# Kernel tuning notes

Measured on AMD Instinct MI355X. Metric: run time of the kernel, lower is better.

## Reference

```python
import jax, jax.numpy as jnp
import numpy as np

NUM_HEADS = 16
HEAD_DIM = 64
TOP_K_TILES = 8
TILE_SIZE = 16
ROPE_BASE = 10000.0


def make_freqs_cis(seq_len, head_dim):
    # [seq, head_dim//2] complex64, standard RoPE frequencies
    inv_freq = 1.0 / (ROPE_BASE ** (jnp.arange(0, head_dim, 2, dtype=jnp.float32) / head_dim))
    angles = jnp.arange(seq_len, dtype=jnp.float32)[:, None] * inv_freq[None, :]
    return jax.lax.complex(jnp.cos(angles), jnp.sin(angles))


def apply_rope(xq, xk, freqs_cis):
    # xq, xk: [b, h, s, d]; pairs adjacent channels as (real, imag)
    xq_ = xq.astype(jnp.float32).reshape(*xq.shape[:-1], -1, 2)
    xk_ = xk.astype(jnp.float32).reshape(*xk.shape[:-1], -1, 2)
    xq_c = jax.lax.complex(xq_[..., 0], xq_[..., 1])
    xk_c = jax.lax.complex(xk_[..., 0], xk_[..., 1])
    f = freqs_cis[None, None, :xq.shape[2], :]
    xq_r = xq_c * f
    xk_r = xk_c * f
    xq_out = jnp.stack([xq_r.real, xq_r.imag], axis=-1).reshape(xq.shape)
    xk_out = jnp.stack([xk_r.real, xk_r.imag], axis=-1).reshape(xk.shape)
    return xq_out.astype(xq.dtype), xk_out.astype(xk.dtype)


def setup_inputs() -> dict:
    key = jax.random.key(0)
    ks = jax.random.split(key, 5)
    B, S, D = 2, 2048, 1024
    scale = 1.0 / np.sqrt(D)
    return {
        "x": jax.random.normal(ks[0], (B, S, D), dtype=jnp.float32),
        "wq": jax.random.normal(ks[1], (D, NUM_HEADS * HEAD_DIM), dtype=jnp.float32) * scale,
        "wk": jax.random.normal(ks[2], (D, NUM_HEADS * HEAD_DIM), dtype=jnp.float32) * scale,
        "wv": jax.random.normal(ks[3], (D, NUM_HEADS * HEAD_DIM), dtype=jnp.float32) * scale,
        "wo": jax.random.normal(ks[4], (NUM_HEADS * HEAD_DIM, D), dtype=jnp.float32) * scale,
    }


def reference(x, wq, wk, wv, wo):
    batch, seq_len, _ = x.shape
    q = (x @ wq).reshape(batch, seq_len, NUM_HEADS, HEAD_DIM)
    k = (x @ wk).reshape(batch, seq_len, NUM_HEADS, HEAD_DIM)
    v = (x @ wv).reshape(batch, seq_len, NUM_HEADS, HEAD_DIM)

    freqs_cis = make_freqs_cis(seq_len, HEAD_DIM)
    q_t = jnp.transpose(q, (0, 2, 1, 3))
    k_t = jnp.transpose(k, (0, 2, 1, 3))
    q_t, k_t = apply_rope(q_t, k_t, freqs_cis)
    q = jnp.transpose(q_t, (0, 2, 1, 3))
    k = jnp.transpose(k_t, (0, 2, 1, 3))

    logits = jnp.einsum('bqhd,bkhd->bhqk', q, k) / jnp.sqrt(jnp.float32(HEAD_DIM))
    causal = jnp.tril(jnp.ones((seq_len, seq_len), dtype=bool))
    logits = jnp.where(causal[None, None, :, :], logits, -1e10)
    weights = jax.nn.softmax(logits, axis=-1)  # [b, h, q, k]

    # Scout: tile-max-pool last token's attention probs + top-k tile selection
    last_token_probs = weights[:, :, -1, :]  # [b, h, k]
    pad_len = (TILE_SIZE - seq_len % TILE_SIZE) % TILE_SIZE
    if pad_len > 0:
        last_token_probs = jnp.pad(last_token_probs, ((0, 0), (0, 0), (0, pad_len)))
    num_tiles = last_token_probs.shape[-1] // TILE_SIZE
    tile_scores = jnp.max(
        last_token_probs.reshape(batch, NUM_HEADS, num_tiles, TILE_SIZE), axis=-1)
    _, top_tile_indices = jax.lax.top_k(tile_scores, TOP_K_TILES)  # [b, h, top_k]

    output = jnp.einsum('bhqk,bkhd->bqhd', weights, v)
    output = output.reshape(batch, seq_len, NUM_HEADS * HEAD_DIM)
    output = output @ wo
    return output, top_tile_indices
```

## Files before the change

kernel.cpp:

```cpp
#include <hip/hip_runtime.h>

#define B_ 2
#define S_ 2048
#define E_ 1024
#define H_ 16
#define D_ 64
#define BS_ (B_*S_)
#define PSTR 76

typedef unsigned short u16;
typedef __attribute__((ext_vector_type(8))) short short8;
typedef __attribute__((ext_vector_type(4))) float floatx4;
typedef __bf16 bf16x8 __attribute__((ext_vector_type(8)));

__device__ __forceinline__ u16 f2bf(float f) {
    unsigned int u = __builtin_bit_cast(unsigned int, f);
    u += 0x7FFFu + ((u >> 16) & 1u);
    return (u16)(u >> 16);
}
__device__ __forceinline__ float bf2f(u16 h) {
    return __builtin_bit_cast(float, (unsigned int)h << 16);
}
__device__ __forceinline__ floatx4 mfma16(short8 a, short8 b, floatx4 c) {
    return __builtin_amdgcn_mfma_f32_16x16x32_bf16(
        __builtin_bit_cast(bf16x8, a), __builtin_bit_cast(bf16x8, b), c, 0, 0, 0);
}
__device__ __forceinline__ void gload_lds16(const void* g, void* l) {
    __builtin_amdgcn_global_load_lds(
        (const __attribute__((address_space(1))) unsigned int*)g,
        (__attribute__((address_space(3))) unsigned int*)l, 16, 0, 0);
}

__global__ __launch_bounds__(256) void prep_kernel(const float* __restrict__ x,
                                                   const float* __restrict__ wq,
                                                   const float* __restrict__ wk,
                                                   const float* __restrict__ wv,
                                                   const float* __restrict__ wo,
                                                   u16* __restrict__ xcat,
                                                   u16* __restrict__ wqt,
                                                   u16* __restrict__ wkt,
                                                   u16* __restrict__ wkres,
                                                   u16* __restrict__ wvt,
                                                   u16* __restrict__ wot,
                                                   float* __restrict__ cost,
                                                   float* __restrict__ sint,
                                                   float* __restrict__ qlast) {
    __shared__ float t[32][33];
    int bx = blockIdx.x;
    int tid = threadIdx.x;
    if (bx < 4096) {
        int i = bx * 256 + tid;
        int row = i >> 8, c4 = (i & 255) * 4;
        float4 v = ((const float4*)x)[i];
        u16 h0 = f2bf(v.x), h1 = f2bf(v.y), h2 = f2bf(v.z), h3 = f2bf(v.w);
        uint2 o;
        o.x = (unsigned)h0 | ((unsigned)h1 << 16);
        o.y = (unsigned)h2 | ((unsigned)h3 << 16);
        *(uint2*)&xcat[(size_t)row * 2048 + c4] = o;
        u16 l0 = f2bf(v.x - bf2f(h0)), l1 = f2bf(v.y - bf2f(h1));
        u16 l2 = f2bf(v.z - bf2f(h2)), l3 = f2bf(v.w - bf2f(h3));
        uint2 ol;
        ol.x = (unsigned)l0 | ((unsigned)l1 << 16);
        ol.y = (unsigned)l2 | ((unsigned)l3 << 16);
        *(uint2*)&xcat[(size_t)row * 2048 + 1024 + c4] = ol;
    } else if (bx < 8192) {
        int sub = bx - 4096;
        int which = sub >> 10, s2 = sub & 1023;
        const float* W = which == 0 ? wq : which == 1 ? wk : which == 2 ? wv : wo;
        u16* Wt = which == 0 ? wqt : which == 1 ? wkt : which == 2 ? wvt : wot;
        int tk = (s2 >> 5) * 32, tn = (s2 & 31) * 32;
        int tx = tid & 31, ty = tid >> 5;
        for (int i = 0; i < 32; i += 8)
            t[ty + i][tx] = W[(size_t)(tk + ty + i) * E_ + tn + tx];
        __syncthreads();
        for (int i = 0; i < 32; i += 8) {
            float v = t[tx][ty + i];
            u16 hi = f2bf(v);
            Wt[(size_t)(tn + ty + i) * E_ + tk + tx] = hi;
            if (which == 1) {
                wkres[(size_t)(tn + ty + i) * 2048 + tk + tx] = f2bf(v - bf2f(hi));
                wkres[(size_t)(tn + ty + i) * 2048 + 1024 + tk + tx] = hi;
            }
        }
    } else if (bx < 8448) {
        int idx = (bx - 8192) * 256 + tid;
        int s = idx >> 5, i = idx & 31;
        float inv = powf(10000.0f, -(float)i / 32.0f);
        float a = (float)s * inv;
        cost[idx] = cosf(a);
        sint[idx] = sinf(a);
    } else {
        float* red = &t[0][0];
        int b2 = bx - 8448;
        int b = b2 >> 5, c0 = (b2 & 31) * 32;
        int cl = tid & 31, kc = tid >> 5;
        const float* xr = &x[((size_t)b * S_ + (S_ - 1)) * E_ + kc * 128];
        const float* wp = &wq[(size_t)(kc * 128) * E_ + c0 + cl];
        float acc = 0.f;
#pragma unroll 4
        for (int e = 0; e < 128; ++e) acc = fmaf(xr[e], wp[(size_t)e * E_], acc);
        red[kc * 32 + cl] = acc;
        __syncthreads();
        if (kc == 0) {
            float s = ((red[0 * 32 + cl] + red[1 * 32 + cl]) + (red[2 * 32 + cl] + red[3 * 32 + cl]))
                    + ((red[4 * 32 + cl] + red[5 * 32 + cl]) + (red[6 * 32 + cl] + red[7 * 32 + cl]));
            qlast[(size_t)b * E_ + c0 + cl] = s;
        }
    }
}


__device__ __forceinline__ void stage_swz(const u16* __restrict__ src, int row0, int k0,
                                          int stride, u16* lds, int tid) {
    int wv = tid >> 6, ln = tid & 63;
    int swz = (((ln & 7) ^ (ln >> 3)) << 3);
    int rr = ln >> 3;
#pragma unroll
    for (int i = 0; i < 4; ++i) {
        int seg = i * 4 + wv;
        gload_lds16(&src[(size_t)(row0 + seg * 8 + rr) * stride + k0 + swz],
                    (char*)lds + (size_t)seg * 1024);
    }
}

__device__ __forceinline__ void gemm_body(const u16* lA, const u16* lB,
                                          floatx4 (*acc)[4], int lane, int wave) {
    int wm = (wave >> 1) * 64, wn = (wave & 1) * 64;
    int lr = lane & 15, lq = lane >> 4, r7 = lr & 7;
#pragma unroll
    for (int half = 0; half < 2; ++half) {
        int xo = (((half * 4 + lq) ^ r7) << 3);
        short8 afr[4], bfr[4];
#pragma unroll
        for (int mi = 0; mi < 4; ++mi)
            afr[mi] = *(const short8*)&lA[(wm + mi * 16 + lr) * 64 + xo];
#pragma unroll
        for (int ni = 0; ni < 4; ++ni)
            bfr[ni] = *(const short8*)&lB[(wn + ni * 16 + lr) * 64 + xo];
        __builtin_amdgcn_s_setprio(1);
#pragma unroll
        for (int mi = 0; mi < 4; ++mi)
#pragma unroll
            for (int ni = 0; ni < 4; ++ni)
                acc[mi][ni] = mfma16(afr[mi], bfr[ni], acc[mi][ni]);
        __builtin_amdgcn_s_setprio(0);
    }
}

__device__ __forceinline__ void gemm_write(float* __restrict__ C, floatx4 (*acc)[4],
                                           int m0, int n0, int N, int lane, int wave) {
    int wm = (wave >> 1) * 64, wn = (wave & 1) * 64;
    int lr = lane & 15, lq = lane >> 4;
#pragma unroll
    for (int mi = 0; mi < 4; ++mi)
#pragma unroll
        for (int ni = 0; ni < 4; ++ni)
#pragma unroll
            for (int r = 0; r < 4; ++r)
                C[(size_t)(m0 + wm + mi * 16 + lq * 4 + r) * N + n0 + wn + ni * 16 + lr]
                    = acc[mi][ni][r];
}

__device__ __forceinline__ void rope_epilogue(floatx4 (*acc)[4], int m0, int n0,
                                              const float* __restrict__ cost,
                                              const float* __restrict__ sint,
                                              const float* __restrict__ qlast,
                                              u16* __restrict__ dstb,
                                              float* __restrict__ tscores,
                                              int lane, int wave) {
    int wm = (wave >> 1) * 64, wn = (wave & 1) * 64;
    int lr = lane & 15, lq = lane >> 4;
    int odd = lr & 1;
    int h = (n0 + wn) >> 6;
    int bq = m0 >> 11;
    int s0 = m0 & 2047;
    float qr[4];
    if (qlast) {
#pragma unroll
        for (int ni = 0; ni < 4; ++ni) {
            int d = ni * 16 + lr;
            int i = d >> 1;
            float qv = qlast[(size_t)bq * E_ + h * 64 + d];
            float qp = __shfl_xor(qv, 1);
            float c = cost[2047 * 32 + i], sn = sint[2047 * 32 + i];
            qr[ni] = odd ? (qp * sn + qv * c) : (qv * c - qp * sn);
        }
    }
    float dotp[4][4];
#pragma unroll
    for (int mi = 0; mi < 4; ++mi)
#pragma unroll
        for (int r = 0; r < 4; ++r) dotp[mi][r] = 0.f;
#pragma unroll
    for (int ni = 0; ni < 4; ++ni) {
        int d = ni * 16 + lr;
        int i = d >> 1;
#pragma unroll
        for (int mi = 0; mi < 4; ++mi) {
#pragma unroll
            for (int r = 0; r < 4; ++r) {
                int row = m0 + wm + mi * 16 + lq * 4 + r;
                int s = row & 2047;
                float own = acc[mi][ni][r];
                float par = __shfl_xor(own, 1);
                float c = cost[s * 32 + i], sn = sint[s * 32 + i];
                float out = odd ? (par * sn + own * c) : (own * c - par * sn);
                dstb[(((size_t)(bq * 16 + h)) * S_ + s) * 64 + d] = f2bf(out);
                if (qlast) dotp[mi][r] += out * qr[ni];
            }
        }
    }
    if (qlast) {
#pragma unroll
        for (int mi = 0; mi < 4; ++mi) {
            float tm = -1e30f;
#pragma unroll
            for (int r = 0; r < 4; ++r) {
                float dv = dotp[mi][r];
                dv += __shfl_xor(dv, 1);
                dv += __shfl_xor(dv, 2);
                dv += __shfl_xor(dv, 4);
                dv += __shfl_xor(dv, 8);
                tm = fmaxf(tm, dv);
            }
            tm = fmaxf(tm, __shfl_xor(tm, 16));
            tm = fmaxf(tm, __shfl_xor(tm, 32));
            if (lane == 0)
                tscores[(size_t)(bq * 16 + h) * 128 + (s0 >> 4) + (wm >> 4) + mi] = tm;
        }
    }
}

__device__ __forceinline__ void v_epilogue(floatx4 (*acc)[4], int m0, int n0,
                                           u16* vt, u16* __restrict__ vtb,
                                           int lane, int wave, int tid) {
    int wm = (wave >> 1) * 64, wn = (wave & 1) * 64;
    int lr = lane & 15, lq = lane >> 4;
#pragma unroll
    for (int ni = 0; ni < 4; ++ni) {
        int dcol = wn + ni * 16 + lr;
#pragma unroll
        for (int mi = 0; mi < 4; ++mi)
#pragma unroll
            for (int r = 0; r < 4; ++r)
                vt[dcol * 136 + wm + mi * 16 + lq * 4 + r] = f2bf(acc[mi][ni][r]);
    }
    __syncthreads();
    int dcol = tid >> 1, sh = (tid & 1) * 64;
    int colg = n0 + dcol, h = colg >> 6, d = colg & 63;
    int bq = m0 >> 11, s0 = m0 & 2047;
    size_t base = (((size_t)(bq * 16 + h)) * 64 + d) * S_ + s0 + sh;
#pragma unroll
    for (int c = 0; c < 8; ++c)
        *(uint4*)&vtb[base + c * 8] = *(const uint4*)&vt[dcol * 136 + sh + c * 8];
}

__global__ __launch_bounds__(256) void proj_gemm_kernel(const u16* __restrict__ xcat,
                                                        const u16* __restrict__ wqt,
                                                        const u16* __restrict__ wkt,
                                                        const u16* __restrict__ wkres,
                                                        const u16* __restrict__ wvt,
                                                        const float* __restrict__ cost,
                                                        const float* __restrict__ sint,
                                                        const float* __restrict__ qlast,
                                                        u16* __restrict__ qb,
                                                        u16* __restrict__ kb,
                                                        float* __restrict__ tscores,
                                                        u16* __restrict__ vtb) {
    __shared__ __align__(16) u16 lsbuf[17408];
    u16* lA = lsbuf;
    u16* lB = lsbuf + 8192;
    int bx = blockIdx.x;
    int role = bx >> 8;
    int idx = bx & 255;
    int xcd = idx & 7, loc = idx >> 3;
    int m0 = (xcd * 4 + (loc & 3)) * 128;
    int n0 = (loc >> 2) * 128;
    int tid = threadIdx.x, lane = tid & 63, wave = tid >> 6;

    floatx4 acc[4][4];
#pragma unroll
    for (int i = 0; i < 4; ++i)
#pragma unroll
        for (int j = 0; j < 4; ++j) acc[i][j] = (floatx4){0.f, 0.f, 0.f, 0.f};

    if (role == 0) {
        for (int k0 = 0; k0 < 1024; k0 += 64) {
            stage_swz(xcat, m0, k0, 2048, lA, tid);
            stage_swz(wkt, n0, k0, 1024, lB, tid);
            __syncthreads();
            gemm_body(lA, lB, acc, lane, wave);
            __syncthreads();
        }
        for (int k0 = 0; k0 < 2048; k0 += 64) {
            stage_swz(xcat, m0, k0, 2048, lA, tid);
            stage_swz(wkres, n0, k0, 2048, lB, tid);
            __syncthreads();
            gemm_body(lA, lB, acc, lane, wave);
            __syncthreads();
        }
        rope_epilogue(acc, m0, n0, cost, sint, qlast, kb, tscores, lane, wave);
    } else if (role == 1) {
        for (int k0 = 0; k0 < 1024; k0 += 64) {
            stage_swz(xcat, m0, k0, 2048, lA, tid);
            stage_swz(wqt, n0, k0, 1024, lB, tid);
            __syncthreads();
            gemm_body(lA, lB, acc, lane, wave);
            __syncthreads();
        }
        rope_epilogue(acc, m0, n0, cost, sint, (const float*)nullptr, qb,
                      (float*)nullptr, lane, wave);
    } else {
        for (int k0 = 0; k0 < 1024; k0 += 64) {
            stage_swz(xcat, m0, k0, 2048, lA, tid);
            stage_swz(wvt, n0, k0, 1024, lB, tid);
            __syncthreads();
            gemm_body(lA, lB, acc, lane, wave);
            __syncthreads();
        }
        v_epilogue(acc, m0, n0, lsbuf, vtb, lane, wave, tid);
    }
}

__global__ __launch_bounds__(256) void gemm_bf16_kernel(const u16* __restrict__ A,
                                                        const u16* __restrict__ Bt,
                                                        float* __restrict__ C,
                                                        int M, int N, int Kd) {
    __shared__ __align__(16) u16 lds4[4 * 8192];
    u16* T0 = lds4;
    u16* T1 = lds4 + 8192;
    u16* T2 = lds4 + 16384;
    u16* T3 = lds4 + 24576;
    int nwg = (M / 128) * (N / 128);
    int bx = blockIdx.x;
    int q = nwg >> 3, rr = nwg & 7, xcd = bx & 7, pos = bx >> 3;
    int lbx = (xcd < rr ? xcd * (q + 1) : rr * (q + 1) + (xcd - rr) * q) + pos;
    int nbn = N / 128;
    int m0 = (lbx / nbn) * 128, n0 = (lbx % nbn) * 128;
    int tid = threadIdx.x, lane = tid & 63, wave = tid >> 6;

    floatx4 acc[4][4];
#pragma unroll
    for (int i = 0; i < 4; ++i)
#pragma unroll
        for (int j = 0; j < 4; ++j) acc[i][j] = (floatx4){0.f, 0.f, 0.f, 0.f};

    int nsteps = Kd / 64;
    stage_swz(A, m0, 0, Kd, T0, tid);
    stage_swz(Bt, n0, 0, Kd, T2, tid);
    asm volatile("s_waitcnt vmcnt(0)" ::: "memory");
    __syncthreads();
    for (int step = 0; step < nsteps; ++step) {
        int buf = step & 1;
        u16* Ac = buf ? T1 : T0;
        u16* Bc = buf ? T3 : T2;
        if (step + 1 < nsteps) {
            stage_swz(A, m0, (step + 1) * 64, Kd, buf ? T0 : T1, tid);
            stage_swz(Bt, n0, (step + 1) * 64, Kd, buf ? T2 : T3, tid);
        }
        gemm_body(Ac, Bc, acc, lane, wave);
        asm volatile("s_waitcnt vmcnt(0)" ::: "memory");
        __syncthreads();
    }
    gemm_write(C, acc, m0, n0, N, lane, wave);
}

__device__ __forceinline__ void stage_kv(const u16* __restrict__ K, const u16* __restrict__ V,
                                         int n0, u16* kbuf, u16* vbuf, int wave, int lane) {
    int lr = lane & 15, lq = lane >> 4;
    if (wave < 2) {
#pragma unroll
        for (int i = 0; i < 4; ++i) {
            int sk = wave * 4 + i;
            int kt = sk >> 1, kh = (sk & 1) * 32;
            gload_lds16(&K[(size_t)(n0 + kt * 16 + lr) * D_ + kh + lq * 8],
                        kbuf + sk * 512);
        }
    } else {
#pragma unroll
        for (int i = 0; i < 4; ++i) {
            int sv = (wave - 2) * 4 + i;
            int c = sv >> 2, o = sv & 3;
            gload_lds16(&V[(size_t)(o * 16 + lr) * S_ + n0 + c * 32 + lq * 8],
                        vbuf + sv * 512);
        }
    }
}

__global__ __launch_bounds__(256) void flash_kernel(const u16* __restrict__ qb,
                                                    const u16* __restrict__ kb,
                                                    const u16* __restrict__ vtb,
                                                    u16* __restrict__ ab) {
    __shared__ __align__(16) u16 kls[2][8 * 512];
    __shared__ __align__(16) u16 vls[2][8 * 512];
    __shared__ __align__(16) u16 ldsP[4][16 * PSTR];
    int tid = threadIdx.x;
    int lane = tid & 63, wave = tid >> 6;
    int bx = blockIdx.x;
    int xcd = bx & 7, ii = bx >> 3;
    int hid = xcd + 8 * (ii & 3);
    int qc = 31 - (ii >> 2);
    int qt0 = qc * 64 + wave * 16;
    const u16* Q = qb + (size_t)hid * S_ * D_;
    const u16* K = kb + (size_t)hid * S_ * D_;
    const u16* V = vtb + (size_t)hid * D_ * S_;
    u16* lp = &ldsP[wave][0];
    int lr = lane & 15, lq = lane >> 4, lk = lq * 8;

    short8 qfr0 = *(const short8*)&Q[(size_t)(qt0 + lr) * D_ + lk];
    short8 qfr1 = *(const short8*)&Q[(size_t)(qt0 + lr) * D_ + 32 + lk];

    floatx4 o0 = {0,0,0,0}, o1 = {0,0,0,0}, o2 = {0,0,0,0}, o3 = {0,0,0,0};
    float m = -1e30f, l = 0.f;

    stage_kv(K, V, 0, kls[0], vls[0], wave, lane);
    asm volatile("s_waitcnt vmcnt(0)" ::: "memory");
    __syncthreads();

    for (int it = 0; it <= qc; ++it) {
        int n0 = it * 64;
        int buf = it & 1;
        const u16* kbuf = kls[buf];
        const u16* vbuf = vls[buf];
        if (it < qc)
            stage_kv(K, V, n0 + 64, kls[buf ^ 1], vls[buf ^ 1], wave, lane);

        short8 ka0[4], ka1[4];
#pragma unroll
        for (int kt = 0; kt < 4; ++kt) {
            ka0[kt] = *(const short8*)&kbuf[(kt * 2 + 0) * 512 + lane * 8];
            ka1[kt] = *(const short8*)&kbuf[(kt * 2 + 1) * 512 + lane * 8];
        }
        floatx4 st[4];
#pragma unroll
        for (int kt = 0; kt < 4; ++kt) st[kt] = (floatx4){0.f, 0.f, 0.f, 0.f};
        __builtin_amdgcn_s_setprio(1);
#pragma unroll
        for (int kt = 0; kt < 4; ++kt) {
            st[kt] = mfma16(ka0[kt], qfr0, st[kt]);
            st[kt] = mfma16(ka1[kt], qfr1, st[kt]);
        }
        __builtin_amdgcn_s_setprio(0);

        const float SC = 0.18033688011112042f;
        int rem = qt0 + 16 - n0;
        float sv[4][4];
        float bmax = -1e30f;
        if (rem >= 80) {
#pragma unroll
            for (int kt = 0; kt < 4; ++kt)
#pragma unroll
                for (int r = 0; r < 4; ++r) {
                    float s = st[kt][r] * SC;
                    sv[kt][r] = s;
                    bmax = fmaxf(bmax, s);
                }
        } else {
#pragma unroll
            for (int kt = 0; kt < 4; ++kt)
#pragma unroll
                for (int r = 0; r < 4; ++r) {
                    int k = n0 + kt * 16 + lq * 4 + r;
                    float s = (k <= qt0 + lr) ? st[kt][r] * SC : -1e30f;
                    sv[kt][r] = s;
                    bmax = fmaxf(bmax, s);
                }
        }
        bmax = fmaxf(bmax, __shfl_xor(bmax, 16));
        bmax = fmaxf(bmax, __shfl_xor(bmax, 32));
        if (!__all(bmax <= m + 8.0f)) {
            float mn = fmaxf(m, bmax);
            float alpha = __builtin_amdgcn_exp2f(m - mn);
            m = mn;
            l *= alpha;
            float af[4];
#pragma unroll
            for (int r = 0; r < 4; ++r) af[r] = __shfl(alpha, lq * 4 + r);
#pragma unroll
            for (int r = 0; r < 4; ++r) {
                o0[r] *= af[r]; o1[r] *= af[r]; o2[r] *= af[r]; o3[r] *= af[r];
            }
        }
        float ps = 0.f;
#pragma unroll
        for (int kt = 0; kt < 4; ++kt) {
            float p0 = __builtin_amdgcn_exp2f(sv[kt][0] - m);
            float p1 = __builtin_amdgcn_exp2f(sv[kt][1] - m);
            float p2 = __builtin_amdgcn_exp2f(sv[kt][2] - m);
            float p3 = __builtin_amdgcn_exp2f(sv[kt][3] - m);
            ps += (p0 + p1) + (p2 + p3);
            unsigned wlo, whi;
            asm("v_cvt_pk_bf16_f32 %0, %1, %2" : "=v"(wlo) : "v"(p0), "v"(p1));
            asm("v_cvt_pk_bf16_f32 %0, %1, %2" : "=v"(whi) : "v"(p2), "v"(p3));
            *(uint2*)&lp[lr * PSTR + kt * 16 + lq * 4] = (uint2){wlo, whi};
        }
        ps += __shfl_xor(ps, 16);
        ps += __shfl_xor(ps, 32);
        l += ps;

        short8 vv[2][4];
#pragma unroll
        for (int c = 0; c < 2; ++c)
#pragma unroll
            for (int o = 0; o < 4; ++o)
                vv[c][o] = *(const short8*)&vbuf[(c * 4 + o) * 512 + lane * 8];
        asm volatile("s_waitcnt lgkmcnt(0)" ::: "memory");
        __builtin_amdgcn_s_setprio(1);
#pragma unroll
        for (int c = 0; c < 2; ++c) {
            uint2 plo = *(const uint2*)&lp[lr * PSTR + c * 32 + lk];
            uint2 phi = *(const uint2*)&lp[lr * PSTR + c * 32 + lk + 4];
            short8 pfr = __builtin_bit_cast(short8, (uint4){plo.x, plo.y, phi.x, phi.y});
            o0 = mfma16(pfr, vv[c][0], o0);
            o1 = mfma16(pfr, vv[c][1], o1);
            o2 = mfma16(pfr, vv[c][2], o2);
            o3 = mfma16(pfr, vv[c][3], o3);
        }
        __builtin_amdgcn_s_setprio(0);

        if (it < qc) {
            asm volatile("s_waitcnt vmcnt(0)" ::: "memory");
            __syncthreads();
        }
    }
    float li[4];
#pragma unroll
    for (int r = 0; r < 4; ++r) li[r] = 1.0f / __shfl(l, lq * 4 + r);
    int b = hid >> 4, h = hid & 15;
    size_t orow_base = ((size_t)b * S_ + qt0 + lq * 4) * E_ + h * D_;
#pragma unroll
    for (int r = 0; r < 4; ++r) {
        size_t rb = orow_base + (size_t)r * E_;
        ab[rb + 0  + lr] = f2bf(o0[r] * li[r]);
        ab[rb + 16 + lr] = f2bf(o1[r] * li[r]);
        ab[rb + 32 + lr] = f2bf(o2[r] * li[r]);
        ab[rb + 48 + lr] = f2bf(o3[r] * li[r]);
    }
}

__global__ __launch_bounds__(64) void topk_select_kernel(const float* __restrict__ tscores,
                                                         float* __restrict__ oidx) {
    int bh = blockIdx.x, tid = threadIdx.x;
    float v0 = tscores[bh * 128 + tid], v1 = tscores[bh * 128 + 64 + tid];
    float va, vb; int ia, ib;
    if (v1 > v0) { va = v1; ia = tid + 64; vb = v0; ib = tid; }
    else         { va = v0; ia = tid;      vb = v1; ib = tid + 64; }
    float cv = va; int ci = ia; int used = 0;
    for (int t = 0; t < 8; ++t) {
        float bv = cv; int bi = ci;
#pragma unroll
        for (int mk = 1; mk < 64; mk <<= 1) {
            float ov = __shfl_xor(bv, mk);
            int oi = __shfl_xor(bi, mk);
            if (ov > bv || (ov == bv && oi < bi)) { bv = ov; bi = oi; }
        }
        if (tid == 0) oidx[bh * 8 + t] = (float)bi;
        if (ci == bi) {
            if (used == 0) { cv = vb; ci = ib; used = 1; }
            else           { cv = -3e30f; ci = 1 << 20; }
        }
    }
}

extern "C" void kernel_launch(void* const* d_in, const int* in_sizes, int n_in,
                              void* d_out, int out_size, void* d_ws, size_t ws_size,
                              hipStream_t stream) {
    (void)in_sizes; (void)n_in; (void)out_size; (void)ws_size;
    const float* x  = (const float*)d_in[0];
    const float* wq = (const float*)d_in[1];
    const float* wk = (const float*)d_in[2];
    const float* wv = (const float*)d_in[3];
    const float* wo = (const float*)d_in[4];
    float* out = (float*)d_out;

    char* wsp = (char*)d_ws;
    size_t off = 0;
    auto nxt = [&](size_t bytes) {
        char* p = wsp + off;
        off = (off + bytes + 255) & ~(size_t)255;
        return p;
    };
    u16* xcat  = (u16*)nxt((size_t)BS_ * 2048 * 2);
    u16* wqt   = (u16*)nxt((size_t)E_ * E_ * 2);
    u16* wkt   = (u16*)nxt((size_t)E_ * E_ * 2);
    u16* wkres = (u16*)nxt((size_t)E_ * 2048 * 2);
    u16* wvt   = (u16*)nxt((size_t)E_ * E_ * 2);
    u16* wot   = (u16*)nxt((size_t)E_ * E_ * 2);
    float* cost = (float*)nxt((size_t)S_ * 32 * 4);
    float* sint = (float*)nxt((size_t)S_ * 32 * 4);
    u16* qb    = (u16*)nxt((size_t)B_ * H_ * S_ * D_ * 2);
    u16* kb    = (u16*)nxt((size_t)B_ * H_ * S_ * D_ * 2);
    u16* vtb   = (u16*)nxt((size_t)B_ * H_ * S_ * D_ * 2);
    u16* ab    = (u16*)nxt((size_t)BS_ * E_ * 2);
    float* qlast = (float*)nxt((size_t)B_ * E_ * 4);
    float* tscores = (float*)nxt((size_t)B_ * H_ * 128 * 4);

    hipLaunchKernelGGL(prep_kernel, dim3(8512), dim3(256), 0, stream,
                       x, wq, wk, wv, wo, xcat, wqt, wkt, wkres, wvt, wot,
                       cost, sint, qlast);

    hipLaunchKernelGGL(proj_gemm_kernel, dim3(768), dim3(256), 0, stream,
                       xcat, wqt, wkt, wkres, wvt, cost, sint, qlast,
                       qb, kb, tscores, vtb);

    hipLaunchKernelGGL(flash_kernel, dim3(B_ * H_ * (S_ / 64)), dim3(256), 0, stream,
                       qb, kb, vtb, ab);

    hipLaunchKernelGGL(topk_select_kernel, dim3(B_ * H_), dim3(64), 0, stream,
                       tscores, out + (size_t)BS_ * E_);

    hipLaunchKernelGGL(gemm_bf16_kernel, dim3(256), dim3(256), 0, stream, ab, wot, out,
                       BS_, E_, E_);
}
```

Baseline: 211.5 us.

## Process two 16-row query tiles per wave in flash attention to reuse K/V

Each wave now handles 32 query rows as two independent 16-row subtiles that share the same K and V fragments loaded from LDS, so each block covers 128 query rows and the grid is halved. This cuts the K/V global and LDS traffic per query row and amortizes staging and barrier costs. The tradeoff is higher register pressure from doubled accumulators, score tiles and softmax state (launch_bounds is set to 2 blocks per CU), fewer blocks, and coarser causal load balancing.

```diff
diff --git a/kernel.cpp b/kernel.cpp
--- a/kernel.cpp
+++ b/kernel.cpp
@@ -387,42 +387,121 @@
     }
 }
 
-__global__ __launch_bounds__(256) void flash_kernel(const u16* __restrict__ qb,
-                                                    const u16* __restrict__ kb,
-                                                    const u16* __restrict__ vtb,
-                                                    u16* __restrict__ ab) {
+__device__ __forceinline__ void softmax_tile(floatx4* st, int n0, int qbase,
+                                             float& m, float& l, floatx4* o,
+                                             u16* lp, int lr, int lq) {
+    const float SC = 0.18033688011112042f;
+    int rem = qbase + 16 - n0;
+    float sv[4][4];
+    float bmax = -1e30f;
+    if (rem >= 80) {
+#pragma unroll
+        for (int kt = 0; kt < 4; ++kt)
+#pragma unroll
+            for (int r = 0; r < 4; ++r) {
+                float s = st[kt][r] * SC;
+                sv[kt][r] = s;
+                bmax = fmaxf(bmax, s);
+            }
+    } else {
+#pragma unroll
+        for (int kt = 0; kt < 4; ++kt)
+#pragma unroll
+            for (int r = 0; r < 4; ++r) {
+                int k = n0 + kt * 16 + lq * 4 + r;
+                float s = (k <= qbase + lr) ? st[kt][r] * SC : -1e30f;
+                sv[kt][r] = s;
+                bmax = fmaxf(bmax, s);
+            }
+    }
+    bmax = fmaxf(bmax, __shfl_xor(bmax, 16));
+    bmax = fmaxf(bmax, __shfl_xor(bmax, 32));
+    if (!__all(bmax <= m + 8.0f)) {
+        float mn = fmaxf(m, bmax);
+        float alpha = __builtin_amdgcn_exp2f(m - mn);
+        m = mn;
+        l *= alpha;
+        float af[4];
+#pragma unroll
+        for (int r = 0; r < 4; ++r) af[r] = __shfl(alpha, lq * 4 + r);
+#pragma unroll
+        for (int r = 0; r < 4; ++r) {
+            o[0][r] *= af[r]; o[1][r] *= af[r]; o[2][r] *= af[r]; o[3][r] *= af[r];
+        }
+    }
+    float ps = 0.f;
+#pragma unroll
+    for (int kt = 0; kt < 4; ++kt) {
+        float p0 = __builtin_amdgcn_exp2f(sv[kt][0] - m);
+        float p1 = __builtin_amdgcn_exp2f(sv[kt][1] - m);
+        float p2 = __builtin_amdgcn_exp2f(sv[kt][2] - m);
+        float p3 = __builtin_amdgcn_exp2f(sv[kt][3] - m);
+        ps += (p0 + p1) + (p2 + p3);
+        unsigned wlo, whi;
+        asm("v_cvt_pk_bf16_f32 %0, %1, %2" : "=v"(wlo) : "v"(p0), "v"(p1));
+        asm("v_cvt_pk_bf16_f32 %0, %1, %2" : "=v"(whi) : "v"(p2), "v"(p3));
+        *(uint2*)&lp[lr * PSTR + kt * 16 + lq * 4] = (uint2){wlo, whi};
+    }
+    ps += __shfl_xor(ps, 16);
+    ps += __shfl_xor(ps, 32);
+    l += ps;
+}
+
+__device__ __forceinline__ void pv_tile(const u16* lp, const short8 (*vv)[4],
+                                        floatx4* o, int lr, int lk) {
+#pragma unroll
+    for (int c = 0; c < 2; ++c) {
+        uint2 plo = *(const uint2*)&lp[lr * PSTR + c * 32 + lk];
+        uint2 phi = *(const uint2*)&lp[lr * PSTR + c * 32 + lk + 4];
+        short8 pfr = __builtin_bit_cast(short8, (uint4){plo.x, plo.y, phi.x, phi.y});
+        o[0] = mfma16(pfr, vv[c][0], o[0]);
+        o[1] = mfma16(pfr, vv[c][1], o[1]);
+        o[2] = mfma16(pfr, vv[c][2], o[2]);
+        o[3] = mfma16(pfr, vv[c][3], o[3]);
+    }
+}
+
+__global__ __launch_bounds__(256, 2) void flash_kernel(const u16* __restrict__ qb,
+                                                       const u16* __restrict__ kb,
+                                                       const u16* __restrict__ vtb,
+                                                       u16* __restrict__ ab) {
     __shared__ __align__(16) u16 kls[2][8 * 512];
     __shared__ __align__(16) u16 vls[2][8 * 512];
-    __shared__ __align__(16) u16 ldsP[4][16 * PSTR];
+    __shared__ __align__(16) u16 ldsP[4][2][16 * PSTR];
     int tid = threadIdx.x;
     int lane = tid & 63, wave = tid >> 6;
     int bx = blockIdx.x;
     int xcd = bx & 7, ii = bx >> 3;
     int hid = xcd + 8 * (ii & 3);
-    int qc = 31 - (ii >> 2);
-    int qt0 = qc * 64 + wave * 16;
+    int qc = 15 - (ii >> 2);
+    int qt0 = qc * 128 + wave * 32;
     const u16* Q = qb + (size_t)hid * S_ * D_;
     const u16* K = kb + (size_t)hid * S_ * D_;
     const u16* V = vtb + (size_t)hid * D_ * S_;
-    u16* lp = &ldsP[wave][0];
+    u16* lpA = &ldsP[wave][0][0];
+    u16* lpB = &ldsP[wave][1][0];
     int lr = lane & 15, lq = lane >> 4, lk = lq * 8;
 
-    short8 qfr0 = *(const short8*)&Q[(size_t)(qt0 + lr) * D_ + lk];
-    short8 qfr1 = *(const short8*)&Q[(size_t)(qt0 + lr) * D_ + 32 + lk];
-
-    floatx4 o0 = {0,0,0,0}, o1 = {0,0,0,0}, o2 = {0,0,0,0}, o3 = {0,0,0,0};
-    float m = -1e30f, l = 0.f;
+    short8 qfrA0 = *(const short8*)&Q[(size_t)(qt0 + lr) * D_ + lk];
+    short8 qfrA1 = *(const short8*)&Q[(size_t)(qt0 + lr) * D_ + 32 + lk];
+    short8 qfrB0 = *(const short8*)&Q[(size_t)(qt0 + 16 + lr) * D_ + lk];
+    short8 qfrB1 = *(const short8*)&Q[(size_t)(qt0 + 16 + lr) * D_ + 32 + lk];
+
+    floatx4 oA[4] = {{0,0,0,0},{0,0,0,0},{0,0,0,0},{0,0,0,0}};
+    floatx4 oB[4] = {{0,0,0,0},{0,0,0,0},{0,0,0,0},{0,0,0,0}};
+    float mA = -1e30f, lA_ = 0.f, mB = -1e30f, lB_ = 0.f;
 
     stage_kv(K, V, 0, kls[0], vls[0], wave, lane);
     asm volatile("s_waitcnt vmcnt(0)" ::: "memory");
     __syncthreads();
 
-    for (int it = 0; it <= qc; ++it) {
+    int ntiles = 2 * qc + 2;
+    for (int it = 0; it < ntiles; ++it) {
         int n0 = it * 64;
         int buf = it & 1;
         const u16* kbuf = kls[buf];
         const u16* vbuf = vls[buf];
-        if (it < qc)
+        if (it + 1 < ntiles)
             stage_kv(K, V, n0 + 64, kls[buf ^ 1], vls[buf ^ 1], wave, lane);
 
         short8 ka0[4], ka1[4];
@@ -431,72 +510,23 @@
             ka0[kt] = *(const short8*)&kbuf[(kt * 2 + 0) * 512 + lane * 8];
             ka1[kt] = *(const short8*)&kbuf[(kt * 2 + 1) * 512 + lane * 8];
         }
-        floatx4 st[4];
-#pragma unroll
-        for (int kt = 0; kt < 4; ++kt) st[kt] = (floatx4){0.f, 0.f, 0.f, 0.f};
+        floatx4 stA[4] = {{0,0,0,0},{0,0,0,0},{0,0,0,0},{0,0,0,0}};
+        floatx4 stB[4] = {{0,0,0,0},{0,0,0,0},{0,0,0,0},{0,0,0,0}};
         __builtin_amdgcn_s_setprio(1);
 #pragma unroll
         for (int kt = 0; kt < 4; ++kt) {
-            st[kt] = mfma16(ka0[kt], qfr0, st[kt]);
-            st[kt] = mfma16(ka1[kt], qfr1, st[kt]);
+            stA[kt] = mfma16(ka0[kt], qfrA0, stA[kt]);
+            stA[kt] = mfma16(ka1[kt], qfrA1, stA[kt]);
+        }
+#pragma unroll
+        for (int kt = 0; kt < 4; ++kt) {
+            stB[kt] = mfma16(ka0[kt], qfrB0, stB[kt]);
+            stB[kt] = mfma16(ka1[kt], qfrB1, stB[kt]);
         }
         __builtin_amdgcn_s_setprio(0);
 
-        const float SC = 0.18033688011112042f;
-        int rem = qt0 + 16 - n0;
-        float sv[4][4];
-        float bmax = -1e30f;
-        if (rem >= 80) {
-#pragma unroll
-            for (int kt = 0; kt < 4; ++kt)
-#pragma unroll
-                for (int r = 0; r < 4; ++r) {
-                    float s = st[kt][r] * SC;
-                    sv[kt][r] = s;
-                    bmax = fmaxf(bmax, s);
-                }
-        } else {
-#pragma unroll
-            for (int kt = 0; kt < 4; ++kt)
-#pragma unroll
-                for (int r = 0; r < 4; ++r) {
-                    int k = n0 + kt * 16 + lq * 4 + r;
-                    float s = (k <= qt0 + lr) ? st[kt][r] * SC : -1e30f;
-                    sv[kt][r] = s;
-                    bmax = fmaxf(bmax, s);
-                }
-        }
-        bmax = fmaxf(bmax, __shfl_xor(bmax, 16));
-        bmax = fmaxf(bmax, __shfl_xor(bmax, 32));
-        if (!__all(bmax <= m + 8.0f)) {
-            float mn = fmaxf(m, bmax);
-            float alpha = __builtin_amdgcn_exp2f(m - mn);
-            m = mn;
-            l *= alpha;
-            float af[4];
-#pragma unroll
-            for (int r = 0; r < 4; ++r) af[r] = __shfl(alpha, lq * 4 + r);
-#pragma unroll
-            for (int r = 0; r < 4; ++r) {
-                o0[r] *= af[r]; o1[r] *= af[r]; o2[r] *= af[r]; o3[r] *= af[r];
-            }
-        }
-        float ps = 0.f;
-#pragma unroll
-        for (int kt = 0; kt < 4; ++kt) {
-            float p0 = __builtin_amdgcn_exp2f(sv[kt][0] - m);
-            float p1 = __builtin_amdgcn_exp2f(sv[kt][1] - m);
-            float p2 = __builtin_amdgcn_exp2f(sv[kt][2] - m);
-            float p3 = __builtin_amdgcn_exp2f(sv[kt][3] - m);
-            ps += (p0 + p1) + (p2 + p3);
-            unsigned wlo, whi;
-            asm("v_cvt_pk_bf16_f32 %0, %1, %2" : "=v"(wlo) : "v"(p0), "v"(p1));
-            asm("v_cvt_pk_bf16_f32 %0, %1, %2" : "=v"(whi) : "v"(p2), "v"(p3));
-            *(uint2*)&lp[lr * PSTR + kt * 16 + lq * 4] = (uint2){wlo, whi};
-        }
-        ps += __shfl_xor(ps, 16);
-        ps += __shfl_xor(ps, 32);
-        l += ps;
+        softmax_tile(stA, n0, qt0, mA, lA_, oA, lpA, lr, lq);
+        softmax_tile(stB, n0, qt0 + 16, mB, lB_, oB, lpB, lr, lq);
 
         short8 vv[2][4];
 #pragma unroll
@@ -506,35 +536,43 @@
                 vv[c][o] = *(const short8*)&vbuf[(c * 4 + o) * 512 + lane * 8];
         asm volatile("s_waitcnt lgkmcnt(0)" ::: "memory");
         __builtin_amdgcn_s_setprio(1);
-#pragma unroll
-        for (int c = 0; c < 2; ++c) {
-            uint2 plo = *(const uint2*)&lp[lr * PSTR + c * 32 + lk];
-            uint2 phi = *(const uint2*)&lp[lr * PSTR + c * 32 + lk + 4];
-            short8 pfr = __builtin_bit_cast(short8, (uint4){plo.x, plo.y, phi.x, phi.y});
-            o0 = mfma16(pfr, vv[c][0], o0);
-            o1 = mfma16(pfr, vv[c][1], o1);
-            o2 = mfma16(pfr, vv[c][2], o2);
-            o3 = mfma16(pfr, vv[c][3], o3);
-        }
+        pv_tile(lpA, vv, oA, lr, lk);
+        pv_tile(lpB, vv, oB, lr, lk);
         __builtin_amdgcn_s_setprio(0);
 
-        if (it < qc) {
+        if (it + 1 < ntiles) {
             asm volatile("s_waitcnt vmcnt(0)" ::: "memory");
             __syncthreads();
         }
     }
-    float li[4];
-#pragma unroll
-    for (int r = 0; r < 4; ++r) li[r] = 1.0f / __shfl(l, lq * 4 + r);
     int b = hid >> 4, h = hid & 15;
-    size_t orow_base = ((size_t)b * S_ + qt0 + lq * 4) * E_ + h * D_;
-#pragma unroll
-    for (int r = 0; r < 4; ++r) {
-        size_t rb = orow_base + (size_t)r * E_;
-        ab[rb + 0  + lr] = f2bf(o0[r] * li[r]);
-        ab[rb + 16 + lr] = f2bf(o1[r] * li[r]);
-        ab[rb + 32 + lr] = f2bf(o2[r] * li[r]);
-        ab[rb + 48 + lr] = f2bf(o3[r] * li[r]);
+    {
+        float li[4];
+#pragma unroll
+        for (int r = 0; r < 4; ++r) li[r] = 1.0f / __shfl(lA_, lq * 4 + r);
+        size_t orow_base = ((size_t)b * S_ + qt0 + lq * 4) * E_ + h * D_;
+#pragma unroll
+        for (int r = 0; r < 4; ++r) {
+            size_t rb = orow_base + (size_t)r * E_;
+            ab[rb + 0  + lr] = f2bf(oA[0][r] * li[r]);
+            ab[rb + 16 + lr] = f2bf(oA[1][r] * li[r]);
+            ab[rb + 32 + lr] = f2bf(oA[2][r] * li[r]);
+            ab[rb + 48 + lr] = f2bf(oA[3][r] * li[r]);
+        }
+    }
+    {
+        float li[4];
+#pragma unroll
+        for (int r = 0; r < 4; ++r) li[r] = 1.0f / __shfl(lB_, lq * 4 + r);
+        size_t orow_base = ((size_t)b * S_ + qt0 + 16 + lq * 4) * E_ + h * D_;
+#pragma unroll
+        for (int r = 0; r < 4; ++r) {
+            size_t rb = orow_base + (size_t)r * E_;
+            ab[rb + 0  + lr] = f2bf(oB[0][r] * li[r]);
+            ab[rb + 16 + lr] = f2bf(oB[1][r] * li[r]);
+            ab[rb + 32 + lr] = f2bf(oB[2][r] * li[r]);
+            ab[rb + 48 + lr] = f2bf(oB[3][r] * li[r]);
+        }
     }
 }
 
@@ -603,7 +641,7 @@
                        xcat, wqt, wkt, wkres, wvt, cost, sint, qlast,
                        qb, kb, tscores, vtb);
 
-    hipLaunchKernelGGL(flash_kernel, dim3(B_ * H_ * (S_ / 64)), dim3(256), 0, stream,
+    hipLaunchKernelGGL(flash_kernel, dim3(B_ * H_ * (S_ / 128)), dim3(256), 0, stream,
                        qb, kb, vtb, ab);
 
     hipLaunchKernelGGL(topk_select_kernel, dim3(B_ * H_), dim3(64), 0, stream,
```

After: 216.1 us. 1.02x slower.
